# Kernel optimization log

Measured on AMD Instinct MI355X. Metric: run time of the kernel, lower is better.

Reference implementation:

```python
import jax, jax.numpy as jnp
import numpy as np

T, N = 20, 32768          # seq_length, numNodes
D_IN, D_EMB, D_H, D_OUT = 2, 64, 128, 5


def setup_inputs() -> dict:
    key = jax.random.key(0)
    ks = jax.random.split(key, 12)
    s = 0.05
    return {
        "nodes": jax.random.normal(ks[0], (T, N, D_IN), jnp.float32),
        "present_mask": jax.random.randint(ks[1], (T, N), 0, 2).astype(bool),
        "hidden_states": jax.random.normal(ks[2], (N, D_H), jnp.float32),
        "cell_states": jax.random.normal(ks[3], (N, D_H), jnp.float32),
        "W_embed": jax.random.normal(ks[4], (D_IN, D_EMB), jnp.float32) * s,
        "b_embed": jnp.zeros((D_EMB,), jnp.float32),
        "W_ih": jax.random.normal(ks[5], (D_EMB, 4 * D_H), jnp.float32) * s,
        "b_ih": jnp.zeros((4 * D_H,), jnp.float32),
        "W_hh": jax.random.normal(ks[6], (D_H, 4 * D_H), jnp.float32) * s,
        "b_hh": jnp.zeros((4 * D_H,), jnp.float32),
        "W_out": jax.random.normal(ks[7], (D_H, D_OUT), jnp.float32) * s,
        "b_out": jnp.zeros((D_OUT,), jnp.float32),
    }


def reference(nodes, present_mask, hidden_states, cell_states,
              W_embed, b_embed, W_ih, b_ih, W_hh, b_hh, W_out, b_out):
    # Per-frame: gather present nodes -> embed+ReLU (dropout=eval identity)
    # -> LSTMCell -> scatter h/c/output back. Gather+scatter is expressed as
    # a masked update, which is mathematically identical.
    def step(carry, frame):
        h, c = carry
        x, mask = frame                      # x: [N,2], mask: [N]
        emb = jax.nn.relu(x @ W_embed + b_embed)              # [N,Demb]
        gates = emb @ W_ih + b_ih + h @ W_hh + b_hh           # [N,4H]
        i, f, g, o = jnp.split(gates, 4, axis=-1)             # torch order
        i, f, o = jax.nn.sigmoid(i), jax.nn.sigmoid(f), jax.nn.sigmoid(o)
        g = jnp.tanh(g)
        c_new = f * c + i * g
        h_new = o * jnp.tanh(c_new)
        m = mask[:, None]
        h = jnp.where(m, h_new, h)
        c = jnp.where(m, c_new, c)
        out = jnp.where(m, h_new @ W_out + b_out, 0.0)        # absent -> zeros
        return (h, c), out

    (h_fin, c_fin), outputs = jax.lax.scan(
        step, (hidden_states, cell_states), (nodes, present_mask))
    return outputs, h_fin, c_fin                              # [T,N,5],[N,H],[N,H]
```

## Files before the change

### kernel.cpp

```cpp
#include <hip/hip_runtime.h>
#include <cstddef>


typedef __attribute__((ext_vector_type(8))) short  s16x8;
typedef __attribute__((ext_vector_type(4))) float  f32x4;

namespace {
constexpr int T_STEPS = 20;
constexpr int NN      = 32768;
constexpr int D_EMB   = 64;
constexpr int D_H     = 128;
constexpr int D_OUT   = 5;
constexpr int G4      = 512;
constexpr int MT      = 64;
constexpr int BLOCK   = 512;
constexpr int GRID    = NN / MT;
constexpr int WP_ELEMS   = 8 * 4 * 6 * 64 * 8;
constexpr int WOUT_ELEMS = 4 * 64 * 8;
constexpr int HSTR    = 136;
constexpr float LOG2E = 1.4426950408889634f;
constexpr float AM4   = -4.0f * LOG2E;
constexpr float AP2   =  2.0f * LOG2E;
constexpr float CINV  = 0.34657359027997264f;
constexpr size_t OFF_H = (size_t)T_STEPS * NN * D_OUT;
constexpr size_t OFF_C = OFF_H + (size_t)NN * D_H;
}

__device__ __forceinline__ unsigned short f2bf(float x) {
    unsigned u = __float_as_uint(x);
    u = (u + 0x7FFFu + ((u >> 16) & 1u)) >> 16;
    return (unsigned short)u;
}
__device__ __forceinline__ unsigned short f2bf_hw(float x) {
    __bf16 b = (__bf16)x;
    union { __bf16 b; unsigned short u; } cv;
    cv.b = b;
    return cv.u;
}
__device__ __forceinline__ float bf2f(unsigned short h) {
    return __uint_as_float(((unsigned)h) << 16);
}
__device__ __forceinline__ float exp2f_fast(float x) {
#if __has_builtin(__builtin_amdgcn_exp2f)
    return __builtin_amdgcn_exp2f(x);
#else
    return __expf(x * 0.6931471805599453f);
#endif
}
__device__ __forceinline__ float sig_pre(float a) {
    return __builtin_amdgcn_rcpf(1.0f + exp2f_fast(a));
}

__global__ void prepack_kernel(const float* __restrict__ W_ih,
                               const float* __restrict__ b_ih,
                               const float* __restrict__ W_hh,
                               const float* __restrict__ b_hh,
                               const float* __restrict__ W_out,
                               unsigned short* __restrict__ Wp,
                               unsigned short* __restrict__ WoutF,
                               float* __restrict__ b_sum) {
    int idx = blockIdx.x * blockDim.x + threadIdx.x;
    if (idx < WP_ELEMS) {
        int j    = idx & 7;
        int L    = (idx >> 3) & 63;
        int rest = idx >> 9;
        int kb   = rest % 6;
        int gw   = rest / 6;
        int g    = gw & 3, w = gw >> 2;
        int k    = kb * 32 + (L >> 4) * 8 + j;
        int col  = g * D_H + w * 16 + (L & 15);
        float v  = (k < D_EMB) ? W_ih[k * G4 + col] : W_hh[(k - D_EMB) * G4 + col];
        float s  = (g == 2) ? (2.0f * LOG2E) : (-LOG2E);
        Wp[idx] = f2bf(v * s);
    } else if (idx < WP_ELEMS + WOUT_ELEMS) {
        int i2 = idx - WP_ELEMS;
        int j = i2 & 7, L = (i2 >> 3) & 63, kb2 = i2 >> 9;
        int k = kb2 * 32 + (L >> 4) * 8 + j;
        int n = L & 15;
        WoutF[i2] = (n < D_OUT) ? f2bf(W_out[k * D_OUT + n]) : (unsigned short)0;
    }
    if (idx < G4) {
        int g = idx / D_H;
        float s = (g == 2) ? (2.0f * LOG2E) : (-LOG2E);
        b_sum[idx] = (b_ih[idx] + b_hh[idx]) * s;
    }
}

__global__ __launch_bounds__(BLOCK, 1) void vlstm_kernel(
    const float* __restrict__ nodes,
    const int*   __restrict__ mask,
    const float* __restrict__ h0,
    const float* __restrict__ c0,
    const float* __restrict__ W_embed,
    const float* __restrict__ b_embed,
    const float* __restrict__ b_out,
    const unsigned short* __restrict__ Wp,
    const unsigned short* __restrict__ WoutF,
    const float* __restrict__ b_sum,
    float* __restrict__ out)
{
    __shared__ __align__(16) unsigned short E[2][4 * 2 * 512];
    __shared__ __align__(16) unsigned short hNewC[2][4 * 4 * 512];
    __shared__ float          cS[MT * 132];
    __shared__ __align__(16) unsigned short hS[MT * HSTR];
    __shared__ float          st_o[2][MT * D_OUT];
    __shared__ __align__(16) unsigned short WoS[WOUT_ELEMS];
    __shared__ float We_s[2 * D_EMB];
    __shared__ float be_s[D_EMB];
    __shared__ unsigned long long msk64[2];
    __shared__ unsigned char lst[2][MT];
    __shared__ int nAs[2];

    const int tid  = threadIdx.x;
    const int wave = tid >> 6;
    const int L    = tid & 63;
    const int quad = L >> 4;
    const int l15  = L & 15;
    const int n_base = blockIdx.x * MT;
    const int u_lane = wave * 16 + l15;

    const unsigned short* wbase = Wp + (size_t)wave * (4 * 6 * 64 * 8);
    s16x8 Bf[4][6];
    #pragma unroll
    for (int g = 0; g < 4; g++)
        #pragma unroll
        for (int kb = 0; kb < 6; kb++)
            Bf[g][kb] = *(const s16x8*)(wbase + ((g * 6 + kb) * 64 + L) * 8);

    float bias[4];
    #pragma unroll
    for (int g = 0; g < 4; g++) bias[g] = b_sum[g * D_H + u_lane];
    const float bo = (l15 < D_OUT) ? b_out[l15] : 0.0f;

    const int kbu2 = u_lane >> 5;
    const int j_u  = u_lane & 7;
    const int flh  = ((u_lane >> 3) & 3) * 128 + quad * 32;
    const int node_e = tid >> 3;
    const int eb     = tid & 7;

    for (int i = tid; i < 3 * D_EMB; i += BLOCK) {
        if (i < 2 * D_EMB) We_s[i] = W_embed[i];
        else               be_s[i - 2 * D_EMB] = b_embed[i - 2 * D_EMB];
    }
    for (int i = tid; i < WOUT_ELEMS; i += BLOCK) WoS[i] = WoutF[i];

    for (int i = tid; i < MT * D_H; i += BLOCK) {
        int node = i >> 7, u = i & 127;
        cS[node * 132 + u]  = AP2 * c0[(size_t)(n_base + node) * D_H + u];
        hS[node * HSTR + u] = f2bf_hw(h0[(size_t)(n_base + node) * D_H + u]);
    }
    if (wave == 0) {
        int lm0 = mask[n_base + L];
        unsigned long long bm = __ballot(lm0 != 0);
        int na     = __popcll(bm);
        int below  = __popcll(bm & ((1ull << L) - 1ull));
        int belowI = __popcll((~bm) & ((1ull << L) - 1ull));
        lst[0][lm0 ? below : (na + belowI)] = (unsigned char)L;
        if (L == 0) { msk64[0] = bm; nAs[0] = na; }
    }
    __syncthreads();

#define EMB_BUILD(B, XV, MN) do {                                              \
    if (((MN) >> node_e) & 1ull) {                                             \
        int j = __popcll((MN) & ((1ull << node_e) - 1ull));                    \
        s16x8 ev;                                                              \
        _Pragma("unroll")                                                      \
        for (int jj = 0; jj < 8; jj++) {                                       \
            int e = eb * 8 + jj;                                               \
            float v = fmaf((XV).x, We_s[e], fmaf((XV).y, We_s[D_EMB + e], be_s[e])); \
            ev[jj] = (short)f2bf_hw(fmaxf(v, 0.0f));                           \
        }                                                                      \
        *(s16x8*)(&E[B][((j >> 4) * 2 + (eb >> 2)) * 512 + (eb & 3) * 128 + (j & 15) * 8]) = ev; \
    } } while (0)

    {
        float2 x0 = *(const float2*)(nodes + (size_t)(n_base + node_e) * 2);
        unsigned long long M0v = msk64[0];
        EMB_BUILD(0, x0, M0v);
    }
    __syncthreads();

#define GEMM_RT(rt) do {                                                       \
    int og = (int)lstT[(rt) * 16 + l15];                                       \
    const unsigned short* hrow = hS + og * HSTR + quad * 8;                    \
    {   s16x8 af0 = *(const s16x8*)(Er + ((rt) * 2 + 0) * 512 + L * 8);        \
        _Pragma("unroll")                                                      \
        for (int g = 0; g < 4; g++)                                            \
            acc[(rt) & 1][g] = __builtin_amdgcn_mfma_f32_16x16x32_bf16(        \
                af0, Bf[g][0], (f32x4){0.f, 0.f, 0.f, 0.f}, 0, 0, 0); }        \
    {   s16x8 af1 = *(const s16x8*)(Er + ((rt) * 2 + 1) * 512 + L * 8);        \
        _Pragma("unroll")                                                      \
        for (int g = 0; g < 4; g++)                                            \
            acc[(rt) & 1][g] = __builtin_amdgcn_mfma_f32_16x16x32_bf16(        \
                af1, Bf[g][1], acc[(rt) & 1][g], 0, 0, 0); }                   \
    _Pragma("unroll")                                                          \
    for (int kb = 2; kb < 6; kb++) {                                           \
        s16x8 af = *(const s16x8*)(hrow + (kb - 2) * 32);                      \
        _Pragma("unroll")                                                      \
        for (int g = 0; g < 4; g++)                                            \
            acc[(rt) & 1][g] = __builtin_amdgcn_mfma_f32_16x16x32_bf16(        \
                af, Bf[g][kb], acc[(rt) & 1][g], 0, 0, 0); }                   \
} while (0)

#define ACT_RT(rt) do {                                                        \
    _Pragma("unroll")                                                          \
    for (int r = 0; r < 4; r++) {                                              \
        int c    = (rt) * 16 + quad * 4 + r;                                   \
        int orig = (int)lstT[c];                                               \
        float cold = cS[orig * 132 + u_lane];                                  \
        float gi = sig_pre(acc[(rt) & 1][0][r] + bias[0]);                     \
        float gf = sig_pre(acc[(rt) & 1][1][r] + bias[1]);                     \
        float rg = sig_pre(acc[(rt) & 1][2][r] + bias[2]);                     \
        float go = sig_pre(acc[(rt) & 1][3][r] + bias[3]);                     \
        float ggL = fmaf(AM4, rg, AP2);                   \
        float cnL = fmaf(gf, cold, gi * ggL);             \
        float rr  = __builtin_amdgcn_rcpf(1.0f + exp2f_fast(cnL));             \
        float hv  = go * fmaf(-2.0f, rr, 1.0f);           \
        unsigned short hb = f2bf_hw(hv);                                       \
        hbv[rt][r] = hb;                                                       \
        if (c < nA) {                                                          \
            cS[orig * 132 + u_lane] = cnL;                                     \
            hNc[((rt) * 4 + kbu2) * 512 + flh + r * 8 + j_u] = hb;             \
        }                                                                      \
    } } while (0)

    unsigned long long Mp = 0;
    int nAp = 0;

    for (int t = 0; t < T_STEPS; t++) {
        unsigned short* __restrict__ Er   = E[t & 1];
        unsigned short* __restrict__ hNc  = hNewC[t & 1];
        const unsigned short* __restrict__ hPv = hNewC[(t + 1) & 1];
        const unsigned char*  __restrict__ lstT = lst[t & 1];

        const unsigned long long M = msk64[t & 1];
        const int nA  = __builtin_amdgcn_readfirstlane(nAs[t & 1]);
        const int ntA = (nA + 15) >> 4;

        float2 xv = make_float2(0.0f, 0.0f);
        if (t + 1 < T_STEPS) {
            xv = *(const float2*)(nodes + ((size_t)(t + 1) * NN + n_base + node_e) * 2);
            if (wave == 0) {
                int lm = mask[(size_t)(t + 1) * NN + n_base + L];
                unsigned long long bm = __ballot(lm != 0);
                int na     = __popcll(bm);
                int below  = __popcll(bm & ((1ull << L) - 1ull));
                int belowI = __popcll((~bm) & ((1ull << L) - 1ull));
                lst[(t + 1) & 1][lm ? below : (na + belowI)] = (unsigned char)L;
                if (L == 0) { msk64[(t + 1) & 1] = bm; nAs[(t + 1) & 1] = na; }
            }
        }

        f32x4 acc[2][4];
        unsigned short hbv[4][4];
        if (ntA > 0) GEMM_RT(0);
        if (ntA > 1) GEMM_RT(1);
        if (ntA > 0) ACT_RT(0);
        if (ntA > 2) GEMM_RT(2);
        if (ntA > 1) ACT_RT(1);
        if (ntA > 3) GEMM_RT(3);
        if (ntA > 2) ACT_RT(2);
        if (t > 0) {
            int ntP = (nAp + 15) >> 4;
            if (wave < ntP) {
                f32x4 ao = (f32x4){0.f, 0.f, 0.f, 0.f};
                #pragma unroll
                for (int kb2 = 0; kb2 < 4; kb2++) {
                    s16x8 af = *(const s16x8*)(hPv + (wave * 4 + kb2) * 512 + L * 8);
                    s16x8 wf = *(const s16x8*)(WoS + (kb2 * 64 + L) * 8);
                    ao = __builtin_amdgcn_mfma_f32_16x16x32_bf16(af, wf, ao, 0, 0, 0);
                }
                if (l15 < D_OUT) {
                    #pragma unroll
                    for (int r = 0; r < 4; r++) {
                        int c = wave * 16 + quad * 4 + r;
                        st_o[(t - 1) & 1][c * D_OUT + l15] = ao[r] + bo;
                    }
                }
            }
        }
        if (ntA > 3) ACT_RT(3);
        __syncthreads();

        #pragma unroll
        for (int rt = 0; rt < 4; rt++)
            #pragma unroll
            for (int r = 0; r < 4; r++) {
                int c = rt * 16 + quad * 4 + r;
                if (c < nA) hS[(int)lstT[c] * HSTR + u_lane] = hbv[rt][r];
            }
        if (t > 0 && tid < MT * D_OUT) {
            int node = tid / D_OUT, d = tid - node * D_OUT;
            int act  = (int)((Mp >> node) & 1ull);
            int pos  = __popcll(Mp & ((1ull << node) - 1ull));
            float v  = act ? st_o[(t - 1) & 1][pos * D_OUT + d] : 0.0f;
            out[((size_t)(t - 1) * NN + n_base) * D_OUT + tid] = v;
        }
        if (t + 1 < T_STEPS) {
            unsigned long long Mn = msk64[(t + 1) & 1];
            EMB_BUILD((t + 1) & 1, xv, Mn);
        }
        Mp = M; nAp = nA;
        __syncthreads();
    }

    {
        int ntP = (nAp + 15) >> 4;
        if (wave < ntP) {
            const unsigned short* hPv = hNewC[(T_STEPS - 1) & 1];
            f32x4 ao = (f32x4){0.f, 0.f, 0.f, 0.f};
            #pragma unroll
            for (int kb2 = 0; kb2 < 4; kb2++) {
                s16x8 af = *(const s16x8*)(hPv + (wave * 4 + kb2) * 512 + L * 8);
                s16x8 wf = *(const s16x8*)(WoS + (kb2 * 64 + L) * 8);
                ao = __builtin_amdgcn_mfma_f32_16x16x32_bf16(af, wf, ao, 0, 0, 0);
            }
            if (l15 < D_OUT) {
                #pragma unroll
                for (int r = 0; r < 4; r++) {
                    int c = wave * 16 + quad * 4 + r;
                    st_o[(T_STEPS - 1) & 1][c * D_OUT + l15] = ao[r] + bo;
                }
            }
        }
    }
    __syncthreads();
    if (tid < MT * D_OUT) {
        int node = tid / D_OUT, d = tid - node * D_OUT;
        int act  = (int)((Mp >> node) & 1ull);
        int pos  = __popcll(Mp & ((1ull << node) - 1ull));
        float v  = act ? st_o[(T_STEPS - 1) & 1][pos * D_OUT + d] : 0.0f;
        out[((size_t)(T_STEPS - 1) * NN + n_base) * D_OUT + tid] = v;
    }
    for (int i = tid; i < MT * D_H; i += BLOCK) {
        int node = i >> 7, u = i & 127;
        out[OFF_H + (size_t)(n_base + node) * D_H + u] = bf2f(hS[node * HSTR + u]);
        out[OFF_C + (size_t)(n_base + node) * D_H + u] = CINV * cS[node * 132 + u];
    }

#undef EMB_BUILD
#undef GEMM_RT
#undef ACT_RT
}

extern "C" void kernel_launch(void* const* d_in, const int* in_sizes, int n_in,
                              void* d_out, int out_size, void* d_ws, size_t ws_size,
                              hipStream_t stream) {
    const float* nodes   = (const float*)d_in[0];
    const int*   mask    = (const int*)  d_in[1];
    const float* h0      = (const float*)d_in[2];
    const float* c0      = (const float*)d_in[3];
    const float* W_embed = (const float*)d_in[4];
    const float* b_embed = (const float*)d_in[5];
    const float* W_ih    = (const float*)d_in[6];
    const float* b_ih    = (const float*)d_in[7];
    const float* W_hh    = (const float*)d_in[8];
    const float* b_hh    = (const float*)d_in[9];
    const float* W_out   = (const float*)d_in[10];
    const float* b_out   = (const float*)d_in[11];
    float* out = (float*)d_out;

    unsigned short* Wp    = (unsigned short*)d_ws;
    unsigned short* WoutF = Wp + WP_ELEMS;
    float*          b_sum = (float*)(WoutF + WOUT_ELEMS);

    prepack_kernel<<<(WP_ELEMS + WOUT_ELEMS + 255) / 256, 256, 0, stream>>>(
        W_ih, b_ih, W_hh, b_hh, W_out, Wp, WoutF, b_sum);

    vlstm_kernel<<<GRID, BLOCK, 0, stream>>>(
        nodes, mask, h0, c0, W_embed, b_embed, b_out, Wp, WoutF, b_sum, out);
}
```

Before: 270.2 us.

## Drop hNewC staging buffer; compute output projection from hS via compacted index

The per-step staging buffer of new h values, stored in MFMA fragment layout, is removed. The output projection now gathers A fragments straight from the persistent hS array through the previous step's compaction list, which is why the list, mask and count buffers grow to three entries. The bf16 h values held in registers are packed in pairs to cut register pressure. This drops one LDS scatter per activation element and frees LDS, at the cost of gathered, possibly bank-conflicted reads of hS during the projection.

```diff
diff --git a/kernel.cpp b/kernel.cpp
--- a/kernel.cpp
+++ b/kernel.cpp
@@ -100,16 +100,15 @@
     float* __restrict__ out)
 {
     __shared__ __align__(16) unsigned short E[2][4 * 2 * 512];
-    __shared__ __align__(16) unsigned short hNewC[2][4 * 4 * 512];
     __shared__ float          cS[MT * 132];
     __shared__ __align__(16) unsigned short hS[MT * HSTR];
     __shared__ float          st_o[2][MT * D_OUT];
     __shared__ __align__(16) unsigned short WoS[WOUT_ELEMS];
     __shared__ float We_s[2 * D_EMB];
     __shared__ float be_s[D_EMB];
-    __shared__ unsigned long long msk64[2];
-    __shared__ unsigned char lst[2][MT];
-    __shared__ int nAs[2];
+    __shared__ unsigned long long msk64[3];
+    __shared__ unsigned char lst[3][MT];
+    __shared__ int nAs[3];
 
     const int tid  = threadIdx.x;
     const int wave = tid >> 6;
@@ -132,9 +131,6 @@
     for (int g = 0; g < 4; g++) bias[g] = b_sum[g * D_H + u_lane];
     const float bo = (l15 < D_OUT) ? b_out[l15] : 0.0f;
 
-    const int kbu2 = u_lane >> 5;
-    const int j_u  = u_lane & 7;
-    const int flh  = ((u_lane >> 3) & 3) * 128 + quad * 32;
     const int node_e = tid >> 3;
     const int eb     = tid & 7;
 
@@ -216,11 +212,27 @@
         float cnL = fmaf(gf, cold, gi * ggL);             \
         float rr  = __builtin_amdgcn_rcpf(1.0f + exp2f_fast(cnL));             \
         float hv  = go * fmaf(-2.0f, rr, 1.0f);           \
-        unsigned short hb = f2bf_hw(hv);                                       \
-        hbv[rt][r] = hb;                                                       \
-        if (c < nA) {                                                          \
-            cS[orig * 132 + u_lane] = cnL;                                     \
-            hNc[((rt) * 4 + kbu2) * 512 + flh + r * 8 + j_u] = hb;             \
+        unsigned hb = (unsigned)f2bf_hw(hv);                                   \
+        if (r & 1) hbp[rt][r >> 1] |= hb << 16;                                \
+        else       hbp[rt][r >> 1]  = hb;                                      \
+        if (c < nA) cS[orig * 132 + u_lane] = cnL;                             \
+    } } while (0)
+
+#define OPROJ(LSTP, TIDX) do {                                                 \
+    int ogp = (int)(LSTP)[wave * 16 + l15];                                    \
+    const unsigned short* hrp = hS + ogp * HSTR + quad * 8;                    \
+    f32x4 ao = (f32x4){0.f, 0.f, 0.f, 0.f};                                    \
+    _Pragma("unroll")                                                          \
+    for (int kb2 = 0; kb2 < 4; kb2++) {                                        \
+        s16x8 af = *(const s16x8*)(hrp + kb2 * 32);                            \
+        s16x8 wf = *(const s16x8*)(WoS + (kb2 * 64 + L) * 8);                  \
+        ao = __builtin_amdgcn_mfma_f32_16x16x32_bf16(af, wf, ao, 0, 0, 0);     \
+    }                                                                          \
+    if (l15 < D_OUT) {                                                         \
+        _Pragma("unroll")                                                      \
+        for (int r = 0; r < 4; r++) {                                          \
+            int c = wave * 16 + quad * 4 + r;                                  \
+            st_o[(TIDX) & 1][c * D_OUT + l15] = ao[r] + bo;                    \
         }                                                                      \
     } } while (0)
 
@@ -228,13 +240,12 @@
     int nAp = 0;
 
     for (int t = 0; t < T_STEPS; t++) {
-        unsigned short* __restrict__ Er   = E[t & 1];
-        unsigned short* __restrict__ hNc  = hNewC[t & 1];
-        const unsigned short* __restrict__ hPv = hNewC[(t + 1) & 1];
-        const unsigned char*  __restrict__ lstT = lst[t & 1];
-
-        const unsigned long long M = msk64[t & 1];
-        const int nA  = __builtin_amdgcn_readfirstlane(nAs[t & 1]);
+        unsigned short* __restrict__ Er = E[t & 1];
+        const unsigned char* __restrict__ lstT = lst[t % 3];
+        const unsigned char* __restrict__ lstP = lst[(t + 2) % 3];
+
+        const unsigned long long M = msk64[t % 3];
+        const int nA  = __builtin_amdgcn_readfirstlane(nAs[t % 3]);
         const int ntA = (nA + 15) >> 4;
 
         float2 xv = make_float2(0.0f, 0.0f);
@@ -246,13 +257,13 @@
                 int na     = __popcll(bm);
                 int below  = __popcll(bm & ((1ull << L) - 1ull));
                 int belowI = __popcll((~bm) & ((1ull << L) - 1ull));
-                lst[(t + 1) & 1][lm ? below : (na + belowI)] = (unsigned char)L;
-                if (L == 0) { msk64[(t + 1) & 1] = bm; nAs[(t + 1) & 1] = na; }
+                lst[(t + 1) % 3][lm ? below : (na + belowI)] = (unsigned char)L;
+                if (L == 0) { msk64[(t + 1) % 3] = bm; nAs[(t + 1) % 3] = na; }
             }
         }
 
         f32x4 acc[2][4];
-        unsigned short hbv[4][4];
+        unsigned hbp[4][2];
         if (ntA > 0) GEMM_RT(0);
         if (ntA > 1) GEMM_RT(1);
         if (ntA > 0) ACT_RT(0);
@@ -262,22 +273,7 @@
         if (ntA > 2) ACT_RT(2);
         if (t > 0) {
             int ntP = (nAp + 15) >> 4;
-            if (wave < ntP) {
-                f32x4 ao = (f32x4){0.f, 0.f, 0.f, 0.f};
-                #pragma unroll
-                for (int kb2 = 0; kb2 < 4; kb2++) {
-                    s16x8 af = *(const s16x8*)(hPv + (wave * 4 + kb2) * 512 + L * 8);
-                    s16x8 wf = *(const s16x8*)(WoS + (kb2 * 64 + L) * 8);
-                    ao = __builtin_amdgcn_mfma_f32_16x16x32_bf16(af, wf, ao, 0, 0, 0);
-                }
-                if (l15 < D_OUT) {
-                    #pragma unroll
-                    for (int r = 0; r < 4; r++) {
-                        int c = wave * 16 + quad * 4 + r;
-                        st_o[(t - 1) & 1][c * D_OUT + l15] = ao[r] + bo;
-                    }
-                }
-            }
+            if (wave < ntP) OPROJ(lstP, t - 1);
         }
         if (ntA > 3) ACT_RT(3);
         __syncthreads();
@@ -285,9 +281,13 @@
         #pragma unroll
         for (int rt = 0; rt < 4; rt++)
             #pragma unroll
-            for (int r = 0; r < 4; r++) {
-                int c = rt * 16 + quad * 4 + r;
-                if (c < nA) hS[(int)lstT[c] * HSTR + u_lane] = hbv[rt][r];
+            for (int r2 = 0; r2 < 2; r2++) {
+                int c0 = rt * 16 + quad * 4 + r2 * 2;
+                unsigned pk = hbp[rt][r2];
+                if (c0 < nA)
+                    hS[(int)lstT[c0] * HSTR + u_lane] = (unsigned short)(pk & 0xFFFFu);
+                if (c0 + 1 < nA)
+                    hS[(int)lstT[c0 + 1] * HSTR + u_lane] = (unsigned short)(pk >> 16);
             }
         if (t > 0 && tid < MT * D_OUT) {
             int node = tid / D_OUT, d = tid - node * D_OUT;
@@ -297,7 +297,7 @@
             out[((size_t)(t - 1) * NN + n_base) * D_OUT + tid] = v;
         }
         if (t + 1 < T_STEPS) {
-            unsigned long long Mn = msk64[(t + 1) & 1];
+            unsigned long long Mn = msk64[(t + 1) % 3];
             EMB_BUILD((t + 1) & 1, xv, Mn);
         }
         Mp = M; nAp = nA;
@@ -305,24 +305,9 @@
     }
 
     {
+        const unsigned char* __restrict__ lstE = lst[(T_STEPS - 1) % 3];
         int ntP = (nAp + 15) >> 4;
-        if (wave < ntP) {
-            const unsigned short* hPv = hNewC[(T_STEPS - 1) & 1];
-            f32x4 ao = (f32x4){0.f, 0.f, 0.f, 0.f};
-            #pragma unroll
-            for (int kb2 = 0; kb2 < 4; kb2++) {
-                s16x8 af = *(const s16x8*)(hPv + (wave * 4 + kb2) * 512 + L * 8);
-                s16x8 wf = *(const s16x8*)(WoS + (kb2 * 64 + L) * 8);
-                ao = __builtin_amdgcn_mfma_f32_16x16x32_bf16(af, wf, ao, 0, 0, 0);
-            }
-            if (l15 < D_OUT) {
-                #pragma unroll
-                for (int r = 0; r < 4; r++) {
-                    int c = wave * 16 + quad * 4 + r;
-                    st_o[(T_STEPS - 1) & 1][c * D_OUT + l15] = ao[r] + bo;
-                }
-            }
-        }
+        if (wave < ntP) OPROJ(lstE, T_STEPS - 1);
     }
     __syncthreads();
     if (tid < MT * D_OUT) {
@@ -341,6 +326,7 @@
 #undef EMB_BUILD
 #undef GEMM_RT
 #undef ACT_RT
+#undef OPROJ
 }
 
 extern "C" void kernel_launch(void* const* d_in, const int* in_sizes, int n_in,
```

New measurement: 267.5 us. No clear change (-1.0%).
